# Optimization experiments

Hardware: AMD Instinct MI355X
Metric: run time of the kernel (lower is better)

The kernel has to match this reference:

```python
import jax, jax.numpy as jnp
import numpy as np

N, G, F, H, P, OUT = 100000, 64, 64, 128, 2, 2
E = 1_600_000
BN_EPS = 1e-5  # PyG BatchNorm eps; eval mode with running_mean=0, running_var=1


def setup_inputs() -> dict:
    key = jax.random.key(0)
    ks = iter(jax.random.split(key, 64))

    def lin(din, dout):
        w = jax.random.normal(next(ks), (din, dout), jnp.float32) / np.sqrt(din).astype(np.float32)
        return w, jnp.zeros((dout,), jnp.float32)

    inp = {}
    inp["x"] = jax.random.normal(next(ks), (N, F), jnp.float32)
    inp["pos"] = jax.random.normal(next(ks), (N, P), jnp.float32)
    inp["edge_index"] = jax.random.randint(next(ks), (2, E), 0, N, dtype=jnp.int64) if jax.config.jax_enable_x64 else jax.random.randint(next(ks), (2, E), 0, N)
    inp["batch"] = jnp.sort(jax.random.randint(next(ks), (N,), 0, G))
    dims = [F + P, H + P, H + P]
    for l, din in enumerate(dims):
        w1, b1 = lin(din, H)
        w2, b2 = lin(H, H)
        inp[f"w{l}1"], inp[f"b{l}1"] = w1, b1
        inp[f"g{l}1"], inp[f"be{l}1"] = jnp.ones((H,), jnp.float32), jnp.zeros((H,), jnp.float32)
        inp[f"w{l}2"], inp[f"b{l}2"] = w2, b2
        inp[f"g{l}2"], inp[f"be{l}2"] = jnp.ones((H,), jnp.float32), jnp.zeros((H,), jnp.float32)
    inp["wlin"], inp["blin"] = lin(H, OUT)
    return inp


def _bn(h, g, b):
    # eval-mode BatchNorm with running_mean=0, running_var=1
    return h * (g * (1.0 / np.sqrt(1.0 + BN_EPS)).astype(np.float32)) + b


def _mlp(h, w1, b1, g1, be1, w2, b2, g2, be2):
    h = jax.nn.relu(_bn(h @ w1 + b1, g1, be1))
    return jax.nn.relu(_bn(h @ w2 + b2, g2, be2))


def _gin_max(x, src, dst, mlp_params):
    # GINConv with aggr='max', eps=0: mlp(x + max_{j in N(i)} x_j), empty neighborhoods -> 0 (PyG scatter fill)
    agg = jax.ops.segment_max(x[src], dst, num_segments=N)  # [N, C]
    agg = jnp.where(jnp.isneginf(agg), jnp.zeros((), agg.dtype), agg)
    return _mlp(x + agg, *mlp_params)


def reference(x, pos, edge_index, batch,
              w01, b01, g01, be01, w02, b02, g02, be02,
              w11, b11, g11, be11, w12, b12, g12, be12,
              w21, b21, g21, be21, w22, b22, g22, be22,
              wlin, blin):
    src, dst = edge_index[0], edge_index[1]
    h = jnp.concatenate([x, pos], axis=-1)                        # [N, F+P]
    h = _gin_max(h, src, dst, (w01, b01, g01, be01, w02, b02, g02, be02))
    h = jnp.concatenate([h, pos], axis=-1)                        # [N, H+P]
    h = _gin_max(h, src, dst, (w11, b11, g11, be11, w12, b12, g12, be12))
    h = jnp.concatenate([h, pos], axis=-1)
    h = _gin_max(h, src, dst, (w21, b21, g21, be21, w22, b22, g22, be22))
    pooled = jax.ops.segment_max(h, batch, num_segments=G)        # global_max_pool -> [G, H]
    pooled = jnp.where(jnp.isneginf(pooled), jnp.zeros((), pooled.dtype), pooled)
    return pooled @ wlin + blin                                   # logits [G, OUT]
```

## Files before the change

kernel.cpp:

```cpp
#include <hip/hip_runtime.h>
#include <hip/hip_fp16.h>
#include <math.h>
#include <string.h>

constexpr int HDIM = 128;
constexpr int RB   = 136;
constexpr int ZS   = 168;
constexpr float BN_INV = 0.99999500003749980f;

typedef _Float16 half8v __attribute__((ext_vector_type(8)));
typedef __attribute__((ext_vector_type(4))) float float4v;

__device__ __forceinline__ unsigned pkmax(unsigned a, unsigned b) {
  unsigned r;
  asm volatile("v_pk_max_f16 %0, %1, %2" : "=v"(r) : "v"(a), "v"(b));
  return r;
}
__device__ __forceinline__ unsigned pkadd(unsigned a, unsigned b) {
  unsigned r;
  asm volatile("v_pk_add_f16 %0, %1, %2" : "=v"(r) : "v"(a), "v"(b));
  return r;
}

__device__ __forceinline__ float us2f(unsigned short u) { __half h; memcpy(&h, &u, 2); return __half2float(h); }
__device__ __forceinline__ unsigned short f2us(float f) {
  __half h = __float2half(f); unsigned short u; memcpy(&u, &h, 2); return u;
}

__device__ __forceinline__ unsigned encf(float f) {
  unsigned u = __float_as_uint(f);
  return (u & 0x80000000u) ? ~u : (u | 0x80000000u);
}
__device__ __forceinline__ float decf(unsigned u) {
  return (u & 0x80000000u) ? __uint_as_float(u ^ 0x80000000u) : __uint_as_float(~u);
}

__global__ __launch_bounds__(256) void k_bcnt(
    const int* __restrict__ ei, int* __restrict__ chunkHist, int E, int shift) {
  __shared__ int hb[256];
  const int tid = threadIdx.x;
  hb[tid] = 0;
  __syncthreads();
  const int base = blockIdx.x * 4096;
#pragma unroll
  for (int k = 0; k < 16; ++k) {
    int e = base + k * 256 + tid;
    if (e < E) atomicAdd(&hb[ei[E + e] >> shift], 1);
  }
  __syncthreads();
  chunkHist[blockIdx.x * 256 + tid] = hb[tid];
}

__global__ __launch_bounds__(256) void k_bscan(
    const int* __restrict__ chunkHist, int chunks,
    int* __restrict__ bbase, int* __restrict__ gcur, int nbkt, int E) {
  __shared__ int s[256];
  int tid = threadIdx.x;
  int v = 0;
  for (int c = 0; c < chunks; ++c) v += chunkHist[c * 256 + tid];
  s[tid] = v;
  __syncthreads();
  for (int off = 1; off < 256; off <<= 1) {
    int t = (tid >= off) ? s[tid - off] : 0;
    __syncthreads();
    s[tid] += t;
    __syncthreads();
  }
  if (tid < nbkt) {
    int e = s[tid] - v;
    bbase[tid] = e;
    gcur[tid] = e;
  }
  if (tid == 0) bbase[nbkt] = E;
}

__global__ __launch_bounds__(256) void k_bscatter(
    const int* __restrict__ ei, int* __restrict__ gcur,
    unsigned long long* __restrict__ sorted, int E, int shift, int nbkt) {
  __shared__ int hcnt[256];
  __shared__ int hstart[256];
  __shared__ int gbase[256];
  __shared__ unsigned long long sbuf[4096];

  const int tid = threadIdx.x;
  const int base = blockIdx.x * 4096;
  const int validCount = min(4096, E - base);

  hcnt[tid] = 0;
  __syncthreads();

  int sArr[16], dArr[16];
#pragma unroll
  for (int k = 0; k < 16; ++k) {
    int e = base + k * 256 + tid;
    if (e < E) {
      sArr[k] = ei[e];
      dArr[k] = ei[E + e];
      atomicAdd(&hcnt[dArr[k] >> shift], 1);
    } else {
      sArr[k] = -1; dArr[k] = -1;
    }
  }
  __syncthreads();

  {
    int v = hcnt[tid];
    __shared__ int sc[256];
    sc[tid] = v;
    __syncthreads();
    for (int off = 1; off < 256; off <<= 1) {
      int t = (tid >= off) ? sc[tid - off] : 0;
      __syncthreads();
      sc[tid] += t;
      __syncthreads();
    }
    hstart[tid] = sc[tid] - v;
    if (tid < nbkt && v > 0) gbase[tid] = atomicAdd(&gcur[tid], v);
    hcnt[tid] = sc[tid] - v;
  }
  __syncthreads();

#pragma unroll
  for (int k = 0; k < 16; ++k) {
    if (dArr[k] >= 0) {
      int b = dArr[k] >> shift;
      int p = atomicAdd(&hcnt[b], 1);
      sbuf[p] = ((unsigned long long)(unsigned)dArr[k] << 32) | (unsigned)sArr[k];
    }
  }
  __syncthreads();

  for (int p = tid; p < validCount; p += 256) {
    unsigned long long v = sbuf[p];
    int b = (int)(v >> 32) >> shift;
    sorted[(size_t)gbase[b] + (p - hstart[b])] = v;
  }
}

__global__ __launch_bounds__(256) void k_bcsr(
    const unsigned long long* __restrict__ sorted, const int* __restrict__ bbase,
    int* __restrict__ rowptr, int* __restrict__ eidx,
    int shift, int nbkt, int N, int E) {
  __shared__ int cnt[512];
  __shared__ int excl[512];
  __shared__ int sc[256];
  const int b = blockIdx.x, tid = threadIdx.x;
  const int nodeBase = b << shift;
  const int nodesHere = min(512, N - nodeBase);
  const int lo = bbase[b], hi = bbase[b + 1];

  cnt[tid] = 0; cnt[tid + 256] = 0;
  __syncthreads();
  for (int i = lo + tid; i < hi; i += 256) {
    int d = (int)(sorted[i] >> 32);
    atomicAdd(&cnt[d - nodeBase], 1);
  }
  __syncthreads();
  int a0 = cnt[2 * tid], a1 = cnt[2 * tid + 1];
  int pv = a0 + a1;
  sc[tid] = pv;
  __syncthreads();
  for (int off = 1; off < 256; off <<= 1) {
    int t = (tid >= off) ? sc[tid - off] : 0;
    __syncthreads();
    sc[tid] += t;
    __syncthreads();
  }
  int pe = sc[tid] - pv;
  excl[2 * tid] = pe;
  excl[2 * tid + 1] = pe + a0;
  __syncthreads();
  for (int i = tid; i < 512; i += 256) {
    if (i < nodesHere) rowptr[nodeBase + i] = lo + excl[i];
    cnt[i] = excl[i];
  }
  if (b == nbkt - 1 && tid == 0) rowptr[N] = E;
  __syncthreads();
  for (int i = lo + tid; i < hi; i += 256) {
    unsigned long long v = sorted[i];
    int d = (int)(v >> 32);
    int s = (int)(v & 0xFFFFFFFFu);
    int p = atomicAdd(&cnt[d - nodeBase], 1);
    eidx[lo + p] = s;
  }
}

struct PrepArgs {
  const float *x, *pos;
  const float *w01, *w11, *w21, *w02, *w12, *w22;
  const float *b01, *g01, *e01, *b02, *g02, *e02;
  const float *b11, *g11, *e11, *b12, *g12, *e12;
  const float *b21, *g21, *e21, *b22, *g22, *e22;
  unsigned short *h0;
  unsigned short *Wt;
  unsigned *pooled;
  float *Ep;
  int N, GH;
};

__global__ __launch_bounds__(256) void k_prep(PrepArgs a) {
  const int gtid = blockIdx.x * 256 + threadIdx.x;

  if (gtid < a.GH) a.pooled[gtid] = 0x007FFFFFu;

  if (gtid < 61440) {
    int l = gtid / 20480, rem = gtid % 20480;
    int n = rem / 160, k = rem % 160;
    const float* W = (l == 0) ? a.w01 : ((l == 1) ? a.w11 : a.w21);
    int K = (l == 0) ? 66 : 130;
    float v = (k < K) ? W[(size_t)k * 128 + n] : 0.0f;
    a.Wt[gtid] = f2us(v);
  } else if (gtid < 110592) {
    int idx2 = gtid - 61440;
    int l = idx2 / 16384, rem = idx2 % 16384;
    int n = rem / 128, k = rem % 128;
    const float* W = (l == 0) ? a.w02 : ((l == 1) ? a.w12 : a.w22);
    a.Wt[gtid] = f2us(W[(size_t)k * 128 + n]);
  } else if (gtid < 110592 + 768) {
    int idx = gtid - 110592;
    int col = idx & 127, stage = (idx >> 7) & 1, l = idx >> 8;
    const float *bb, *gg, *ee;
    if (l == 0)      { if (!stage) { bb = a.b01; gg = a.g01; ee = a.e01; } else { bb = a.b02; gg = a.g02; ee = a.e02; } }
    else if (l == 1) { if (!stage) { bb = a.b11; gg = a.g11; ee = a.e11; } else { bb = a.b12; gg = a.g12; ee = a.e12; } }
    else             { if (!stage) { bb = a.b21; gg = a.g21; ee = a.e21; } else { bb = a.b22; gg = a.g22; ee = a.e22; } }
    float s = gg[col] * BN_INV;
    a.Ep[l * 512 + stage * 256 + col] = s;
    a.Ep[l * 512 + stage * 256 + 128 + col] = bb[col] * s + ee[col];
  }

  int r = gtid >> 6;
  if (r < a.N) {
    int lane = gtid & 63;
    a.h0[(size_t)r * RB + lane] = f2us(a.x[(size_t)r * 64 + lane]);
    float pv = (lane < 2) ? a.pos[(size_t)r * 2 + lane] : 0.0f;
    a.h0[(size_t)r * RB + 64 + lane] = f2us(pv);
    if (lane < 8) {
      a.h0[(size_t)r * RB + 128 + lane] = f2us((lane < 2) ? a.pos[(size_t)r * 2 + lane] : 0.0f);
    }
  }
}

__global__ __launch_bounds__(256) void k_agg(
    const unsigned short* __restrict__ hcat, const int* __restrict__ rowptr,
    const int* __restrict__ eidx, unsigned short* __restrict__ z,
    int actA, int doTail, int N) {
  int wid = (int)((blockIdx.x * 256 + threadIdx.x) >> 6);
  if (wid >= N) return;
  const int lane = threadIdx.x & 63;
  const int half = lane >> 5;
  const int lc = lane & 31;
  const bool act = (lc < actA) || (doTail && lc == 16);
  const int cb = lc * 8;

  const unsigned NEGINF = 0xFC00FC00u;
  unsigned m0 = NEGINF, m1 = NEGINF, m2 = NEGINF, m3 = NEGINF;

  int r0 = rowptr[wid], r1 = rowptr[wid + 1];
  int e = r0 + half;
  for (; e + 6 < r1; e += 8) {
    int s0 = eidx[e], s1 = eidx[e + 2], s2 = eidx[e + 4], s3 = eidx[e + 6];
    if (act) {
      uint4 v0 = *(const uint4*)(hcat + (size_t)s0 * RB + cb);
      uint4 v1 = *(const uint4*)(hcat + (size_t)s1 * RB + cb);
      uint4 v2 = *(const uint4*)(hcat + (size_t)s2 * RB + cb);
      uint4 v3 = *(const uint4*)(hcat + (size_t)s3 * RB + cb);
      m0 = pkmax(m0, pkmax(pkmax(v0.x, v1.x), pkmax(v2.x, v3.x)));
      m1 = pkmax(m1, pkmax(pkmax(v0.y, v1.y), pkmax(v2.y, v3.y)));
      m2 = pkmax(m2, pkmax(pkmax(v0.z, v1.z), pkmax(v2.z, v3.z)));
      m3 = pkmax(m3, pkmax(pkmax(v0.w, v1.w), pkmax(v2.w, v3.w)));
    }
  }
  for (; e < r1; e += 2) {
    int s = eidx[e];
    if (act) {
      uint4 va = *(const uint4*)(hcat + (size_t)s * RB + cb);
      m0 = pkmax(m0, va.x);
      m1 = pkmax(m1, va.y);
      m2 = pkmax(m2, va.z);
      m3 = pkmax(m3, va.w);
    }
  }

  m0 = pkmax(m0, (unsigned)__shfl_xor((int)m0, 32));
  m1 = pkmax(m1, (unsigned)__shfl_xor((int)m1, 32));
  m2 = pkmax(m2, (unsigned)__shfl_xor((int)m2, 32));
  m3 = pkmax(m3, (unsigned)__shfl_xor((int)m3, 32));

  if (half == 0 && act) {
    if (r0 == r1) { m0 = 0u; m1 = 0u; m2 = 0u; m3 = 0u; }
    uint4 sv = *(const uint4*)(hcat + (size_t)wid * RB + cb);
    uint4 o;
    o.x = pkadd(sv.x, m0);
    o.y = pkadd(sv.y, m1);
    o.z = pkadd(sv.z, m2);
    o.w = pkadd(sv.w, m3);
    *(uint4*)(z + (size_t)wid * RB + cb) = o;
  }
}

__global__ __launch_bounds__(256) void k_mlp(
    const unsigned short* __restrict__ z, int kc1,
    const unsigned short* __restrict__ Wt1, const float* __restrict__ Ep1,
    const unsigned short* __restrict__ Wt2, const float* __restrict__ Ep2,
    unsigned short* __restrict__ out, int N) {
  __shared__ __align__(16) unsigned short zs[4][16][ZS];
  const int tid = threadIdx.x;
  const int w = tid >> 6, lane = tid & 63;
  const int arow = lane & 15;
  const int grp  = lane >> 4;
  const int row0 = blockIdx.x * 64 + w * 16;

  for (int c = lane; c < 16 * 21; c += 64) {
    int r = c / 21, seg = c - r * 21;
    uint4 v = make_uint4(0u, 0u, 0u, 0u);
    if (seg < 17) {
      int gr = row0 + r;
      if (gr >= N) gr = N - 1;
      v = *(const uint4*)(z + (size_t)gr * RB + seg * 8);
    }
    *(uint4*)(&zs[w][r][seg * 8]) = v;
  }

  float4v acc[8];
#pragma unroll
  for (int i = 0; i < 8; ++i) acc[i] = (float4v){0.f, 0.f, 0.f, 0.f};

  for (int kc = 0; kc < kc1; ++kc) {
    half8v a = *(const half8v*)(&zs[w][arow][kc * 32 + grp * 8]);
    const unsigned short* wp = Wt1 + (size_t)arow * 160 + kc * 32 + grp * 8;
#pragma unroll
    for (int nt = 0; nt < 8; ++nt) {
      half8v b = *(const half8v*)(wp + (size_t)(nt * 16) * 160);
      acc[nt] = __builtin_amdgcn_mfma_f32_16x16x32_f16(a, b, acc[nt], 0, 0, 0);
    }
  }

#pragma unroll
  for (int nt = 0; nt < 8; ++nt) {
    int col = nt * 16 + arow;
    float sc = Ep1[col];
    float cc = Ep1[128 + col];
#pragma unroll
    for (int j = 0; j < 4; ++j) {
      float v = fmaxf(fmaf(acc[nt][j], sc, cc), 0.0f);
      zs[w][grp * 4 + j][col] = f2us(v);
    }
  }

#pragma unroll
  for (int i = 0; i < 8; ++i) acc[i] = (float4v){0.f, 0.f, 0.f, 0.f};
  for (int kc = 0; kc < 4; ++kc) {
    half8v a = *(const half8v*)(&zs[w][arow][kc * 32 + grp * 8]);
    const unsigned short* wp = Wt2 + (size_t)arow * HDIM + kc * 32 + grp * 8;
#pragma unroll
    for (int nt = 0; nt < 8; ++nt) {
      half8v b = *(const half8v*)(wp + (size_t)(nt * 16) * HDIM);
      acc[nt] = __builtin_amdgcn_mfma_f32_16x16x32_f16(a, b, acc[nt], 0, 0, 0);
    }
  }

#pragma unroll
  for (int nt = 0; nt < 8; ++nt) {
    int col = nt * 16 + arow;
    float sc = Ep2[col];
    float cc = Ep2[128 + col];
#pragma unroll
    for (int j = 0; j < 4; ++j) {
      int gr = row0 + grp * 4 + j;
      if (gr < N) {
        float v = fmaxf(fmaf(acc[nt][j], sc, cc), 0.0f);
        out[(size_t)gr * RB + col] = f2us(v);
      }
    }
  }
}

__global__ __launch_bounds__(128) void k_pool(
    const unsigned short* __restrict__ hcat, const int* __restrict__ batch,
    unsigned* __restrict__ pooled, int N) {
  int base = blockIdx.x * 128;
  int c = threadIdx.x;
  int end = min(base + 128, N);
  int curg = -1;
  float m = -INFINITY;
  for (int i = base; i < end; ++i) {
    int g = batch[i];
    if (g != curg) {
      if (curg >= 0) atomicMax(&pooled[curg * HDIM + c], encf(m));
      curg = g;
      m = -INFINITY;
    }
    m = fmaxf(m, us2f(hcat[(size_t)i * RB + c]));
  }
  if (curg >= 0) atomicMax(&pooled[curg * HDIM + c], encf(m));
}

__global__ __launch_bounds__(64) void k_final(
    const unsigned* __restrict__ pooled, const float* __restrict__ wlin,
    const float* __restrict__ blin, float* __restrict__ out) {
  int g = blockIdx.x;
  int lane = threadIdx.x;
  float v0 = decf(pooled[g * HDIM + lane]);
  float v1 = decf(pooled[g * HDIM + 64 + lane]);
  if (v0 == -INFINITY) v0 = 0.0f;
  if (v1 == -INFINITY) v1 = 0.0f;
  float p0 = v0 * wlin[lane * 2 + 0] + v1 * wlin[(64 + lane) * 2 + 0];
  float p1 = v0 * wlin[lane * 2 + 1] + v1 * wlin[(64 + lane) * 2 + 1];
  for (int off = 32; off > 0; off >>= 1) {
    p0 += __shfl_down(p0, off);
    p1 += __shfl_down(p1, off);
  }
  if (lane == 0) {
    out[g * 2 + 0] = p0 + blin[0];
    out[g * 2 + 1] = p1 + blin[1];
  }
}

static inline size_t ws_align(size_t x) { return (x + 511) & ~(size_t)511; }

extern "C" void kernel_launch(void* const* d_in, const int* in_sizes, int n_in,
                              void* d_out, int out_size, void* d_ws, size_t ws_size,
                              hipStream_t stream) {
  const float* x     = (const float*)d_in[0];
  const float* pos   = (const float*)d_in[1];
  const int*   ei    = (const int*)d_in[2];
  const int*   batch = (const int*)d_in[3];
  const float* wlin  = (const float*)d_in[28];
  const float* blin  = (const float*)d_in[29];

  const int N = in_sizes[3];
  const int E = in_sizes[2] / 2;
  const int G = out_size / 2;

  int shift = 9;
  while ((((N - 1) >> shift) + 1) > 256) ++shift;
  const int nbkt = ((N - 1) >> shift) + 1;
  const int chunks = (E + 4095) / 4096;

  char* w = (char*)d_ws;
  size_t off = 0;
  auto take = [&](size_t bytes) { void* p = w + off; off += ws_align(bytes); return p; };
  int*            rowptr    = (int*)take((size_t)(N + 1) * 4);
  int*            chunkHist = (int*)take((size_t)chunks * 256 * 4);
  int*            bbase     = (int*)take(2048);
  int*            gcur      = (int*)take(1024);
  int*            eidx      = (int*)take((size_t)E * 4);
  unsigned long long* sorted = (unsigned long long*)take((size_t)E * 8);
  unsigned short* hcat      = (unsigned short*)take((size_t)N * RB * 2 + 1024);
  unsigned short* z         = (unsigned short*)take((size_t)N * RB * 2 + 1024);
  unsigned short* Wt        = (unsigned short*)take((size_t)110592 * 2);
  float*          Ep        = (float*)take(3 * 2 * 2 * 128 * 4);
  unsigned*       pooled    = (unsigned*)take((size_t)G * HDIM * 4);
  (void)ws_size;

  k_bcnt<<<chunks, 256, 0, stream>>>(ei, chunkHist, E, shift);
  k_bscan<<<1, 256, 0, stream>>>(chunkHist, chunks, bbase, gcur, nbkt, E);
  k_bscatter<<<chunks, 256, 0, stream>>>(ei, gcur, sorted, E, shift, nbkt);
  k_bcsr<<<nbkt, 256, 0, stream>>>(sorted, bbase, rowptr, eidx, shift, nbkt, N, E);

  {
    PrepArgs a;
    a.x = x; a.pos = pos;
    a.w01 = (const float*)d_in[4];  a.w11 = (const float*)d_in[12]; a.w21 = (const float*)d_in[20];
    a.w02 = (const float*)d_in[8];  a.w12 = (const float*)d_in[16]; a.w22 = (const float*)d_in[24];
    a.b01 = (const float*)d_in[5];  a.g01 = (const float*)d_in[6];  a.e01 = (const float*)d_in[7];
    a.b02 = (const float*)d_in[9];  a.g02 = (const float*)d_in[10]; a.e02 = (const float*)d_in[11];
    a.b11 = (const float*)d_in[13]; a.g11 = (const float*)d_in[14]; a.e11 = (const float*)d_in[15];
    a.b12 = (const float*)d_in[17]; a.g12 = (const float*)d_in[18]; a.e12 = (const float*)d_in[19];
    a.b21 = (const float*)d_in[21]; a.g21 = (const float*)d_in[22]; a.e21 = (const float*)d_in[23];
    a.b22 = (const float*)d_in[25]; a.g22 = (const float*)d_in[26]; a.e22 = (const float*)d_in[27];
    a.h0 = hcat; a.Wt = Wt; a.pooled = pooled; a.Ep = Ep;
    a.N = N; a.GH = G * HDIM;
    k_prep<<<(N + 3) / 4, 256, 0, stream>>>(a);
  }

  const int actA[3]   = {9, 16, 16};
  const int doTail[3] = {0, 1, 0};
  const int kc1a[3]   = {3, 5, 5};
  const int aggBlocks = (N + 3) / 4;
  const int mlpBlocks = (N + 63) / 64;

  for (int l = 0; l < 3; ++l) {
    const unsigned short* Wt1 = Wt + (size_t)l * 20480;
    const unsigned short* Wt2 = Wt + 61440 + (size_t)l * 16384;
    const float* Ep1 = Ep + l * 512;
    const float* Ep2 = Ep + l * 512 + 256;

    k_agg<<<aggBlocks, 256, 0, stream>>>(hcat, rowptr, eidx, z, actA[l], doTail[l], N);
    k_mlp<<<mlpBlocks, 256, 0, stream>>>(z, kc1a[l], Wt1, Ep1, Wt2, Ep2, hcat, N);
  }

  k_pool<<<(N + 127) / 128, 128, 0, stream>>>(hcat, batch, pooled, N);
  k_final<<<G, 64, 0, stream>>>(pooled, wlin, blin, (float*)d_out);
}
```

Before: 560.5 us.

## Shrink node feature rows to 128 halfs and move pos to a side array

The hidden-feature buffer drops from a 136-half padded row stride to an aligned 128-half stride. The two position values move into a separate packed 32-bit array, which the aggregation kernel max-reduces on a dedicated tail lane and writes into a wider 160-column z buffer for the MLP. Gather traffic and row alignment in the edge-max kernel should improve. Separately, the bucket histogram now accumulates with global atomics into a memset buffer, so the scan no longer loops over per-chunk histograms. The MLP now loads z columns past the written range without zero-filling them, so it relies on zero-padded weights and never-written workspace not holding NaN or Inf.

```diff
diff --git a/kernel.cpp b/kernel.cpp
--- a/kernel.cpp
+++ b/kernel.cpp
@@ -4,7 +4,7 @@
 #include <string.h>
 
 constexpr int HDIM = 128;
-constexpr int RB   = 136;
+constexpr int ZR   = 160;
 constexpr int ZS   = 168;
 constexpr float BN_INV = 0.99999500003749980f;
 
@@ -36,7 +36,7 @@
 }
 
 __global__ __launch_bounds__(256) void k_bcnt(
-    const int* __restrict__ ei, int* __restrict__ chunkHist, int E, int shift) {
+    const int* __restrict__ ei, int* __restrict__ bcnt, int E, int shift, int nbkt) {
   __shared__ int hb[256];
   const int tid = threadIdx.x;
   hb[tid] = 0;
@@ -48,16 +48,15 @@
     if (e < E) atomicAdd(&hb[ei[E + e] >> shift], 1);
   }
   __syncthreads();
-  chunkHist[blockIdx.x * 256 + tid] = hb[tid];
+  if (tid < nbkt && hb[tid] > 0) atomicAdd(&bcnt[tid], hb[tid]);
 }
 
 __global__ __launch_bounds__(256) void k_bscan(
-    const int* __restrict__ chunkHist, int chunks,
-    int* __restrict__ bbase, int* __restrict__ gcur, int nbkt, int E) {
+    const int* __restrict__ bcnt, int* __restrict__ bbase, int* __restrict__ gcur,
+    int nbkt, int E) {
   __shared__ int s[256];
   int tid = threadIdx.x;
-  int v = 0;
-  for (int c = 0; c < chunks; ++c) v += chunkHist[c * 256 + tid];
+  int v = (tid < nbkt) ? bcnt[tid] : 0;
   s[tid] = v;
   __syncthreads();
   for (int off = 1; off < 256; off <<= 1) {
@@ -192,6 +191,7 @@
   const float *b11, *g11, *e11, *b12, *g12, *e12;
   const float *b21, *g21, *e21, *b22, *g22, *e22;
   unsigned short *h0;
+  unsigned *posq;
   unsigned short *Wt;
   unsigned *pooled;
   float *Ep;
@@ -231,70 +231,85 @@
   int r = gtid >> 6;
   if (r < a.N) {
     int lane = gtid & 63;
-    a.h0[(size_t)r * RB + lane] = f2us(a.x[(size_t)r * 64 + lane]);
+    a.h0[(size_t)r * HDIM + lane] = f2us(a.x[(size_t)r * 64 + lane]);
     float pv = (lane < 2) ? a.pos[(size_t)r * 2 + lane] : 0.0f;
-    a.h0[(size_t)r * RB + 64 + lane] = f2us(pv);
-    if (lane < 8) {
-      a.h0[(size_t)r * RB + 128 + lane] = f2us((lane < 2) ? a.pos[(size_t)r * 2 + lane] : 0.0f);
+    a.h0[(size_t)r * HDIM + 64 + lane] = f2us(pv);
+    if (lane == 0) {
+      unsigned p2 = (unsigned)f2us(a.pos[(size_t)r * 2]) |
+                    ((unsigned)f2us(a.pos[(size_t)r * 2 + 1]) << 16);
+      a.posq[r] = p2;
     }
   }
 }
 
 __global__ __launch_bounds__(256) void k_agg(
-    const unsigned short* __restrict__ hcat, const int* __restrict__ rowptr,
-    const int* __restrict__ eidx, unsigned short* __restrict__ z,
-    int actA, int doTail, int N) {
+    const unsigned short* __restrict__ hcat, const unsigned* __restrict__ posq,
+    const int* __restrict__ rowptr, const int* __restrict__ eidx,
+    unsigned short* __restrict__ z, int actA, int doTail, int N) {
   int wid = (int)((blockIdx.x * 256 + threadIdx.x) >> 6);
   if (wid >= N) return;
   const int lane = threadIdx.x & 63;
   const int half = lane >> 5;
   const int lc = lane & 31;
-  const bool act = (lc < actA) || (doTail && lc == 16);
+  const bool act = lc < actA;
+  const bool tail = doTail && (lc == 16);
   const int cb = lc * 8;
 
   const unsigned NEGINF = 0xFC00FC00u;
-  unsigned m0 = NEGINF, m1 = NEGINF, m2 = NEGINF, m3 = NEGINF;
+  unsigned m0 = NEGINF, m1 = NEGINF, m2 = NEGINF, m3 = NEGINF, mt = NEGINF;
 
   int r0 = rowptr[wid], r1 = rowptr[wid + 1];
   int e = r0 + half;
   for (; e + 6 < r1; e += 8) {
     int s0 = eidx[e], s1 = eidx[e + 2], s2 = eidx[e + 4], s3 = eidx[e + 6];
     if (act) {
-      uint4 v0 = *(const uint4*)(hcat + (size_t)s0 * RB + cb);
-      uint4 v1 = *(const uint4*)(hcat + (size_t)s1 * RB + cb);
-      uint4 v2 = *(const uint4*)(hcat + (size_t)s2 * RB + cb);
-      uint4 v3 = *(const uint4*)(hcat + (size_t)s3 * RB + cb);
+      uint4 v0 = *(const uint4*)(hcat + (size_t)s0 * HDIM + cb);
+      uint4 v1 = *(const uint4*)(hcat + (size_t)s1 * HDIM + cb);
+      uint4 v2 = *(const uint4*)(hcat + (size_t)s2 * HDIM + cb);
+      uint4 v3 = *(const uint4*)(hcat + (size_t)s3 * HDIM + cb);
       m0 = pkmax(m0, pkmax(pkmax(v0.x, v1.x), pkmax(v2.x, v3.x)));
       m1 = pkmax(m1, pkmax(pkmax(v0.y, v1.y), pkmax(v2.y, v3.y)));
       m2 = pkmax(m2, pkmax(pkmax(v0.z, v1.z), pkmax(v2.z, v3.z)));
       m3 = pkmax(m3, pkmax(pkmax(v0.w, v1.w), pkmax(v2.w, v3.w)));
     }
+    if (tail) {
+      mt = pkmax(mt, pkmax(pkmax(posq[s0], posq[s1]), pkmax(posq[s2], posq[s3])));
+    }
   }
   for (; e < r1; e += 2) {
     int s = eidx[e];
     if (act) {
-      uint4 va = *(const uint4*)(hcat + (size_t)s * RB + cb);
+      uint4 va = *(const uint4*)(hcat + (size_t)s * HDIM + cb);
       m0 = pkmax(m0, va.x);
       m1 = pkmax(m1, va.y);
       m2 = pkmax(m2, va.z);
       m3 = pkmax(m3, va.w);
     }
+    if (tail) mt = pkmax(mt, posq[s]);
   }
 
   m0 = pkmax(m0, (unsigned)__shfl_xor((int)m0, 32));
   m1 = pkmax(m1, (unsigned)__shfl_xor((int)m1, 32));
   m2 = pkmax(m2, (unsigned)__shfl_xor((int)m2, 32));
   m3 = pkmax(m3, (unsigned)__shfl_xor((int)m3, 32));
-
-  if (half == 0 && act) {
-    if (r0 == r1) { m0 = 0u; m1 = 0u; m2 = 0u; m3 = 0u; }
-    uint4 sv = *(const uint4*)(hcat + (size_t)wid * RB + cb);
-    uint4 o;
-    o.x = pkadd(sv.x, m0);
-    o.y = pkadd(sv.y, m1);
-    o.z = pkadd(sv.z, m2);
-    o.w = pkadd(sv.w, m3);
-    *(uint4*)(z + (size_t)wid * RB + cb) = o;
+  mt = pkmax(mt, (unsigned)__shfl_xor((int)mt, 32));
+
+  if (half == 0) {
+    const bool none = (r0 == r1);
+    if (act) {
+      if (none) { m0 = 0u; m1 = 0u; m2 = 0u; m3 = 0u; }
+      uint4 sv = *(const uint4*)(hcat + (size_t)wid * HDIM + cb);
+      uint4 o;
+      o.x = pkadd(sv.x, m0);
+      o.y = pkadd(sv.y, m1);
+      o.z = pkadd(sv.z, m2);
+      o.w = pkadd(sv.w, m3);
+      *(uint4*)(z + (size_t)wid * ZR + cb) = o;
+    }
+    if (tail) {
+      if (none) mt = 0u;
+      *(unsigned*)(z + (size_t)wid * ZR + 128) = pkadd(posq[wid], mt);
+    }
   }
 }
 
@@ -310,14 +325,11 @@
   const int grp  = lane >> 4;
   const int row0 = blockIdx.x * 64 + w * 16;
 
-  for (int c = lane; c < 16 * 21; c += 64) {
-    int r = c / 21, seg = c - r * 21;
-    uint4 v = make_uint4(0u, 0u, 0u, 0u);
-    if (seg < 17) {
-      int gr = row0 + r;
-      if (gr >= N) gr = N - 1;
-      v = *(const uint4*)(z + (size_t)gr * RB + seg * 8);
-    }
+  for (int c = lane; c < 16 * 20; c += 64) {
+    int r = c / 20, seg = c - r * 20;
+    int gr = row0 + r;
+    if (gr >= N) gr = N - 1;
+    uint4 v = *(const uint4*)(z + (size_t)gr * ZR + seg * 8);
     *(uint4*)(&zs[w][r][seg * 8]) = v;
   }
 
@@ -369,7 +381,7 @@
       int gr = row0 + grp * 4 + j;
       if (gr < N) {
         float v = fmaxf(fmaf(acc[nt][j], sc, cc), 0.0f);
-        out[(size_t)gr * RB + col] = f2us(v);
+        out[(size_t)gr * HDIM + col] = f2us(v);
       }
     }
   }
@@ -390,7 +402,7 @@
       curg = g;
       m = -INFINITY;
     }
-    m = fmaxf(m, us2f(hcat[(size_t)i * RB + c]));
+    m = fmaxf(m, us2f(hcat[(size_t)i * HDIM + c]));
   }
   if (curg >= 0) atomicMax(&pooled[curg * HDIM + c], encf(m));
 }
@@ -440,21 +452,23 @@
   char* w = (char*)d_ws;
   size_t off = 0;
   auto take = [&](size_t bytes) { void* p = w + off; off += ws_align(bytes); return p; };
-  int*            rowptr    = (int*)take((size_t)(N + 1) * 4);
-  int*            chunkHist = (int*)take((size_t)chunks * 256 * 4);
-  int*            bbase     = (int*)take(2048);
-  int*            gcur      = (int*)take(1024);
-  int*            eidx      = (int*)take((size_t)E * 4);
+  int*            rowptr = (int*)take((size_t)(N + 1) * 4);
+  int*            bcnt   = (int*)take(1024);
+  int*            bbase  = (int*)take(2048);
+  int*            gcur   = (int*)take(1024);
+  int*            eidx   = (int*)take((size_t)E * 4);
   unsigned long long* sorted = (unsigned long long*)take((size_t)E * 8);
-  unsigned short* hcat      = (unsigned short*)take((size_t)N * RB * 2 + 1024);
-  unsigned short* z         = (unsigned short*)take((size_t)N * RB * 2 + 1024);
-  unsigned short* Wt        = (unsigned short*)take((size_t)110592 * 2);
-  float*          Ep        = (float*)take(3 * 2 * 2 * 128 * 4);
-  unsigned*       pooled    = (unsigned*)take((size_t)G * HDIM * 4);
+  unsigned short* hcat   = (unsigned short*)take((size_t)N * HDIM * 2);
+  unsigned*       posq   = (unsigned*)take((size_t)N * 4);
+  unsigned short* z      = (unsigned short*)take((size_t)N * ZR * 2);
+  unsigned short* Wt     = (unsigned short*)take((size_t)110592 * 2);
+  float*          Ep     = (float*)take(3 * 2 * 2 * 128 * 4);
+  unsigned*       pooled = (unsigned*)take((size_t)G * HDIM * 4);
   (void)ws_size;
 
-  k_bcnt<<<chunks, 256, 0, stream>>>(ei, chunkHist, E, shift);
-  k_bscan<<<1, 256, 0, stream>>>(chunkHist, chunks, bbase, gcur, nbkt, E);
+  hipMemsetAsync(bcnt, 0, 1024, stream);
+  k_bcnt<<<chunks, 256, 0, stream>>>(ei, bcnt, E, shift, nbkt);
+  k_bscan<<<1, 256, 0, stream>>>(bcnt, bbase, gcur, nbkt, E);
   k_bscatter<<<chunks, 256, 0, stream>>>(ei, gcur, sorted, E, shift, nbkt);
   k_bcsr<<<nbkt, 256, 0, stream>>>(sorted, bbase, rowptr, eidx, shift, nbkt, N, E);
 
@@ -469,7 +483,7 @@
     a.b12 = (const float*)d_in[17]; a.g12 = (const float*)d_in[18]; a.e12 = (const float*)d_in[19];
     a.b21 = (const float*)d_in[21]; a.g21 = (const float*)d_in[22]; a.e21 = (const float*)d_in[23];
     a.b22 = (const float*)d_in[25]; a.g22 = (const float*)d_in[26]; a.e22 = (const float*)d_in[27];
-    a.h0 = hcat; a.Wt = Wt; a.pooled = pooled; a.Ep = Ep;
+    a.h0 = hcat; a.posq = posq; a.Wt = Wt; a.pooled = pooled; a.Ep = Ep;
     a.N = N; a.GH = G * HDIM;
     k_prep<<<(N + 3) / 4, 256, 0, stream>>>(a);
   }
@@ -486,7 +500,8 @@
     const float* Ep1 = Ep + l * 512;
     const float* Ep2 = Ep + l * 512 + 256;
 
-    k_agg<<<aggBlocks, 256, 0, stream>>>(hcat, rowptr, eidx, z, actA[l], doTail[l], N);
+    k_agg<<<aggBlocks, 256, 0, stream>>>(hcat, posq, rowptr, eidx, z,
+                                         actA[l], doTail[l], N);
     k_mlp<<<mlpBlocks, 256, 0, stream>>>(z, kc1a[l], Wt1, Ep1, Wt2, Ep2, hcat, N);
   }
 
```

New measurement: 518.6 us. 7.5% less time.
